# Optimization experiments

Hardware: AMD Instinct MI355X
Metric: run time of the kernel (lower is better)

Reference implementation:

```python
import jax, jax.numpy as jnp
import numpy as np

HEADS = 8
DIM_HEAD = 32
EPS = 1e-5


def setup_inputs() -> dict:
    key = jax.random.key(0)
    ks = jax.random.split(key, 6)
    B, C, N = 2, 256, 2048
    inner = HEADS * DIM_HEAD  # 256
    return {
        "x": jax.random.normal(ks[0], (B, C, N), dtype=jnp.float32),
        "gamma": jnp.ones((C,), dtype=jnp.float32),
        "beta": jnp.zeros((C,), dtype=jnp.float32),
        "wk": jax.random.normal(ks[1], (inner, C // HEADS), dtype=jnp.float32) * 0.05,
        "wq": jax.random.normal(ks[2], (inner, C // HEADS), dtype=jnp.float32) * 0.05,
        "wv": jax.random.normal(ks[3], (inner, C // HEADS), dtype=jnp.float32) * 0.05,
        "wo": jax.random.normal(ks[4], (C, inner), dtype=jnp.float32) * 0.05,
        "bo": jnp.zeros((C,), dtype=jnp.float32),
    }


def reference(x, gamma, beta, wk, wq, wv, wo, bo):
    B, C, N = x.shape
    inner = HEADS * DIM_HEAD
    # BatchNorm1d (training mode: batch stats over B and N per channel)
    mean = jnp.mean(x, axis=(0, 2), keepdims=True)
    var = jnp.mean((x - mean) ** 2, axis=(0, 2), keepdims=True)
    xn = (x - mean) * jax.lax.rsqrt(var + EPS) * gamma[None, :, None] + beta[None, :, None]

    # grouped 1x1 conv1d (groups=HEADS): group g maps C//H input chans -> DIM_HEAD out chans
    xg = xn.reshape(B, HEADS, C // HEADS, N)

    def proj(w):
        w3 = w.reshape(HEADS, DIM_HEAD, C // HEADS)
        return jnp.einsum('hdc,bhcn->bhdn', w3, xg).reshape(B, inner, N)

    k = proj(wk)
    q = proj(wq)
    v = proj(wv)

    # faithful rearrange 'b (d h) n -> b h n d' (d outer, h inner in the channel split)
    def split_heads(t):
        return t.reshape(B, DIM_HEAD, HEADS, N).transpose(0, 2, 3, 1)  # b h n d

    # faithful q/k swap from the original: q<-split(k), k<-split(q), v<-split(v)
    qh, kh, vh = split_heads(k), split_heads(q), split_heads(v)

    scale = DIM_HEAD ** -0.5
    dots = jnp.einsum('bhid,bhjd->bhij', qh, kh) * scale  # [B,H,N,N]
    attn = jax.nn.softmax(dots, axis=-1)
    out = jnp.einsum('bhij,bhjd->bhid', attn, vh)  # [B,H,N,D]

    # rearrange 'b h n d -> b (h d) n'
    out = out.transpose(0, 1, 3, 2).reshape(B, inner, N)
    # output 1x1 conv with bias
    return jnp.einsum('oc,bcn->bon', wo, out) + bo[None, :, None]
```

## Files before the change

kernel.cpp:

```cpp
#include <hip/hip_runtime.h>

#define TID threadIdx.x

constexpr int B = 2, C = 256, N = 2048, H = 8, D = 32, BH = 16;
constexpr float EPS = 1e-5f;
constexpr float SCL2 = 0.25505654344454694f;
constexpr size_t SZ = (size_t)BH * N * D;

typedef _Float16 h8 __attribute__((ext_vector_type(8)));
typedef _Float16 h4 __attribute__((ext_vector_type(4)));
typedef __fp16 fp16x2 __attribute__((ext_vector_type(2)));
typedef float f32x4 __attribute__((ext_vector_type(4)));

__global__ __launch_bounds__(256) void k_bnstats(const float* __restrict__ x,
                                                 const float* __restrict__ gamma,
                                                 const float* __restrict__ beta,
                                                 float* __restrict__ stats) {
  int c = blockIdx.x;
  float s = 0.f, ss = 0.f;
  const float4* x4 = (const float4*)x;
  for (int k = 0; k < B; ++k) {
    const float4* p = x4 + (size_t)(k * C + c) * (N / 4);
    for (int i = TID; i < N / 4; i += 256) {
      float4 v = p[i];
      s += v.x + v.y + v.z + v.w;
      ss += v.x * v.x + v.y * v.y + v.z * v.z + v.w * v.w;
    }
  }
#pragma unroll
  for (int off = 32; off; off >>= 1) {
    s += __shfl_down(s, off);
    ss += __shfl_down(ss, off);
  }
  __shared__ float red[8];
  int w = TID >> 6;
  if ((TID & 63) == 0) { red[w] = s; red[4 + w] = ss; }
  __syncthreads();
  if (TID == 0) {
    float S = red[0] + red[1] + red[2] + red[3];
    float SS = red[4] + red[5] + red[6] + red[7];
    float mean = S * (1.f / (B * N));
    float var = SS * (1.f / (B * N)) - mean * mean;
    float a = rsqrtf(var + EPS) * gamma[c];
    stats[c] = a;
    stats[C + c] = beta[c] - mean * a;
  }
}

__global__ __launch_bounds__(256) void k_proj(const float* __restrict__ x,
    const float* __restrict__ wk, const float* __restrict__ wq,
    const float* __restrict__ wv, const float* __restrict__ stats,
    _Float16* __restrict__ qa, _Float16* __restrict__ ka, _Float16* __restrict__ va) {
  int proj = blockIdx.x >> 8;
  int rem = blockIdx.x & 255;
  int b = rem >> 7;
  int n0 = (rem & 127) * 16;
  const float* w = proj == 0 ? wk : (proj == 1 ? wq : wv);
  _Float16* out = proj == 0 ? qa : (proj == 1 ? ka : va);
  float qs = (proj == 0) ? SCL2 : 1.0f;

  __shared__ float w_t[32 * 264];
  __shared__ float xs[256 * 18];
  __shared__ float sab[512];

  sab[TID] = stats[TID];
  sab[256 + TID] = stats[256 + TID];
  {
    const float4* wr4 = (const float4*)(w + TID * 32);
#pragma unroll
    for (int p = 0; p < 8; ++p) {
      float4 v = wr4[p];
      w_t[(p * 4 + 0) * 264 + TID] = v.x;
      w_t[(p * 4 + 1) * 264 + TID] = v.y;
      w_t[(p * 4 + 2) * 264 + TID] = v.z;
      w_t[(p * 4 + 3) * 264 + TID] = v.w;
    }
  }
  __syncthreads();
#pragma unroll
  for (int p = 0; p < 4; ++p) {
    int c = p * 64 + (TID >> 2);
    int n4 = (TID & 3) * 4;
    float4 v = *(const float4*)(x + (size_t)(b * C + c) * N + n0 + n4);
    float a = sab[c], bb = sab[256 + c];
    int row = (c >> 5) + ((c & 31) << 3);
    int swz = ((row >> 4) & 3) << 2;
    float2 lo = {v.x * a + bb, v.y * a + bb};
    float2 hi = {v.z * a + bb, v.w * a + bb};
    *(float2*)&xs[row * 18 + (n4 ^ swz)] = lo;
    *(float2*)&xs[row * 18 + ((n4 + 2) ^ swz)] = hi;
  }
  __syncthreads();

  int d = TID & 31, t2 = TID >> 5;
  int g = d >> 2;
  float2 acc[8];
#pragma unroll
  for (int h = 0; h < 8; ++h) acc[h] = (float2){0.f, 0.f};
#pragma unroll
  for (int c = 0; c < 32; ++c) {
    float4 w0 = *(const float4*)&w_t[c * 264 + 8 * d];
    float4 w1 = *(const float4*)&w_t[c * 264 + 8 * d + 4];
    int row = g + 8 * c;
    int swz = ((row >> 4) & 3) << 2;
    float2 xv = *(const float2*)&xs[row * 18 + ((t2 * 2) ^ swz)];
    acc[0].x += w0.x * xv.x; acc[0].y += w0.x * xv.y;
    acc[1].x += w0.y * xv.x; acc[1].y += w0.y * xv.y;
    acc[2].x += w0.z * xv.x; acc[2].y += w0.z * xv.y;
    acc[3].x += w0.w * xv.x; acc[3].y += w0.w * xv.y;
    acc[4].x += w1.x * xv.x; acc[4].y += w1.x * xv.y;
    acc[5].x += w1.y * xv.x; acc[5].y += w1.y * xv.y;
    acc[6].x += w1.z * xv.x; acc[6].y += w1.z * xv.y;
    acc[7].x += w1.w * xv.x; acc[7].y += w1.w * xv.y;
  }
  int n = n0 + t2 * 2;
  if (proj < 2) {
#pragma unroll
    for (int h = 0; h < 8; ++h) {
      size_t o = ((size_t)((b * 8 + h) * N) + n) * D + d;
      out[o] = (_Float16)(acc[h].x * qs);
      out[o + D] = (_Float16)(acc[h].y * qs);
    }
  } else {
#pragma unroll
    for (int h = 0; h < 8; ++h) {
      size_t o = ((size_t)((b * 8 + h) * D) + d) * N + n;
      out[o] = (_Float16)acc[h].x;
      out[o + 1] = (_Float16)acc[h].y;
    }
  }
}

__global__ __launch_bounds__(256, 4) void k_attn(
    const _Float16* __restrict__ qa, const _Float16* __restrict__ ka,
    const _Float16* __restrict__ va, float* __restrict__ op,
    float* __restrict__ mp, float* __restrict__ lp) {
  int bid = blockIdx.x;
  int r = bid & 7;
  int q = bid >> 3;
  int js = q >> 6;
  int bh = r * 2 + ((q >> 5) & 1);
  int rb = q & 31;
  constexpr int nst = 8;

  int w = TID >> 6;
  int lane = TID & 63;
  int il = lane & 15;
  int g = lane >> 4;

  __shared__ char Kc[2][8192];
  __shared__ char Vc[2][8192];

  int n_q = rb * 64 + w * 16 + il;
  h8 qf = *(const h8*)(qa + ((size_t)bh * N + n_q) * D + g * 8);

  f32x4 accO0[2], accO1[2];
#pragma unroll
  for (int dh = 0; dh < 2; ++dh) {
    accO0[dh] = (f32x4){0.f, 0.f, 0.f, 0.f};
    accO1[dh] = (f32x4){0.f, 0.f, 0.f, 0.f};
  }
  float m0 = -3.0e38f, l0 = 0.f, m1 = -3.0e38f, l1 = 0.f;

  int kj = TID >> 2, kc = TID & 3;
  int pk = ((kj >> 5) * 2 + ((kj >> 2) & 1)) * 16 + ((kj >> 3) & 3) * 4 + (kj & 3);
  const _Float16* kbase = ka + ((size_t)bh * N + (size_t)js * 1024 + kj) * D + kc * 8;
  int kdst = (pk * 64 + kc * 16) ^ ((pk & 3) << 4);
  int vd = TID >> 3, vc = TID & 7;
  const _Float16* vbase = va + ((size_t)bh * D + vd) * N + (size_t)js * 1024 + vc * 8;
  int vdst = (vd * 128 + vc * 16) ^ ((vd & 7) << 4) ^ (((vd >> 3) & 3) << 5);

  h8 k0 = *(const h8*)kbase;
  h8 k1 = *(const h8*)(kbase + 64 * D);
  h8 v0 = *(const h8*)vbase;
  h8 v1 = *(const h8*)(vbase + 64);
  *(h8*)(Kc[0] + kdst) = k0;
  *(h8*)(Kc[0] + 4096 + kdst) = k1;
  *(h8*)(Vc[0] + vdst) = v0;
  *(h8*)(Vc[0] + 4096 + vdst) = v1;
  __syncthreads();

  auto tile = [&](int cur, int u, float& m, float& l, f32x4* accO) {
    const char* Kt = Kc[cur] + u * 4096;
    const char* Vt = Vc[cur] + u * 4096;
    float pv[4][4];
    float tmax = -3.0e38f;
#pragma unroll
    for (int jt = 0; jt < 4; ++jt) {
      int krow = jt * 16 + il;
      h8 kf = *(const h8*)(Kt + ((krow * 64 + g * 16) ^ ((krow & 3) << 4)));
      f32x4 accS = (f32x4){0.f, 0.f, 0.f, 0.f};
      accS = __builtin_amdgcn_mfma_f32_16x16x32_f16(kf, qf, accS, 0, 0, 0);
#pragma unroll
      for (int e = 0; e < 4; ++e) {
        pv[jt][e] = accS[e];
        tmax = fmaxf(tmax, accS[e]);
      }
    }
    tmax = fmaxf(tmax, __shfl_xor(tmax, 16));
    tmax = fmaxf(tmax, __shfl_xor(tmax, 32));
    if (__any(tmax > m)) {
      float mn = fmaxf(m, tmax);
      float corr = exp2f(m - mn);
      l *= corr;
#pragma unroll
      for (int dh = 0; dh < 2; ++dh)
#pragma unroll
        for (int e = 0; e < 4; ++e) accO[dh][e] *= corr;
      m = mn;
    }
    float ls = 0.f;
#pragma unroll
    for (int jt = 0; jt < 4; ++jt)
#pragma unroll
      for (int e = 0; e < 4; ++e) {
        float pe = exp2f(pv[jt][e] - m);
        pv[jt][e] = pe;
        ls += pe;
      }
    ls += __shfl_xor(ls, 16);
    ls += __shfl_xor(ls, 32);
    l += ls;

#pragma unroll
    for (int jb = 0; jb < 2; ++jb) {
      union { h8 v; fp16x2 p[4]; } u2;
      u2.p[0] = __builtin_amdgcn_cvt_pkrtz(pv[2 * jb][0], pv[2 * jb][1]);
      u2.p[1] = __builtin_amdgcn_cvt_pkrtz(pv[2 * jb][2], pv[2 * jb][3]);
      u2.p[2] = __builtin_amdgcn_cvt_pkrtz(pv[2 * jb + 1][0], pv[2 * jb + 1][1]);
      u2.p[3] = __builtin_amdgcn_cvt_pkrtz(pv[2 * jb + 1][2], pv[2 * jb + 1][3]);
#pragma unroll
      for (int dh = 0; dh < 2; ++dh) {
        int vrow = dh * 16 + il;
        int vaddr = (vrow * 128 + jb * 64 + g * 16) ^ ((vrow & 7) << 4) ^
                    (((vrow >> 3) & 3) << 5);
        h8 vf = *(const h8*)(Vt + vaddr);
        accO[dh] = __builtin_amdgcn_mfma_f32_16x16x32_f16(vf, u2.v, accO[dh], 0, 0, 0);
      }
    }
  };

#pragma unroll
  for (int st = 0; st < nst; ++st) {
    int cur = st & 1;
    bool more = (st + 1 < nst);
    if (more) {
      k0 = *(const h8*)(kbase + (size_t)(st + 1) * 128 * D);
      k1 = *(const h8*)(kbase + (size_t)(st + 1) * 128 * D + 64 * D);
      v0 = *(const h8*)(vbase + (st + 1) * 128);
      v1 = *(const h8*)(vbase + (st + 1) * 128 + 64);
    }

    tile(cur, 0, m0, l0, accO0);
    tile(cur, 1, m1, l1, accO1);

    if (more) {
      *(h8*)(Kc[cur ^ 1] + kdst) = k0;
      *(h8*)(Kc[cur ^ 1] + 4096 + kdst) = k1;
      *(h8*)(Vc[cur ^ 1] + vdst) = v0;
      *(h8*)(Vc[cur ^ 1] + 4096 + vdst) = v1;
      __syncthreads();
    }
  }

  float m = fmaxf(m0, m1);
  float c0 = exp2f(m0 - m), c1 = exp2f(m1 - m);
  float l = l0 * c0 + l1 * c1;
  f32x4 accO[2];
#pragma unroll
  for (int dh = 0; dh < 2; ++dh)
#pragma unroll
    for (int e = 0; e < 4; ++e)
      accO[dh][e] = accO0[dh][e] * c0 + accO1[dh][e] * c1;

  int b = bh >> 3, h = bh & 7;
  size_t obase = ((size_t)((js * 2 + b) * N) + n_q) * C + h * 32;
#pragma unroll
  for (int dh = 0; dh < 2; ++dh) {
    float4 o4 = {accO[dh][0], accO[dh][1], accO[dh][2], accO[dh][3]};
    *(float4*)(op + obase + dh * 16 + g * 4) = o4;
  }
  if (g == 0) {
    size_t idx = (size_t)(js * BH + bh) * N + n_q;
    mp[idx] = m;
    lp[idx] = l;
  }
}

__global__ __launch_bounds__(256) void k_final(const float* __restrict__ op,
    const float* __restrict__ mp, const float* __restrict__ lp,
    const float* __restrict__ wo, const float* __restrict__ bo,
    float* __restrict__ out) {
  __shared__ _Float16 woh[32 * 256];
  __shared__ _Float16 wol[32 * 256];
  __shared__ _Float16 as_[32 * 256];
  __shared__ float cwa[8 * 32], cwb[8 * 32];
  __shared__ float bos[32];
  int nt = blockIdx.x & 63, oq = (blockIdx.x >> 6) & 7, b = blockIdx.x >> 9;
  int n0 = nt * 32, o0 = oq * 32;

  {
    int h = TID >> 5, n_l = TID & 31;
    size_t i0 = (size_t)(b * 8 + h) * N + n0 + n_l;
    size_t i1 = (size_t)(BH + b * 8 + h) * N + n0 + n_l;
    float m0 = mp[i0], m1 = mp[i1];
    float mg = fmaxf(m0, m1);
    float w0 = exp2f(m0 - mg), w1 = exp2f(m1 - mg);
    float inv = 1.f / (w0 * lp[i0] + w1 * lp[i1]);
    cwa[TID] = w0 * inv;
    cwb[TID] = w1 * inv;
  }
  if (TID < 32) bos[TID] = bo[o0 + TID];
  {
    int cc = TID & 63;
    int ob = TID >> 6;
#pragma unroll
    for (int p = 0; p < 8; ++p) {
      int o = ob + p * 4;
      float4 v = ((const float4*)wo)[(o0 + o) * 64 + cc];
      _Float16 h0 = (_Float16)v.x, h1 = (_Float16)v.y,
               h2c = (_Float16)v.z, h3 = (_Float16)v.w;
      h4 hi = {h0, h1, h2c, h3};
      h4 lo = {(_Float16)(v.x - (float)h0), (_Float16)(v.y - (float)h1),
               (_Float16)(v.z - (float)h2c), (_Float16)(v.w - (float)h3)};
      int byte = (o * 512 + cc * 8) ^ ((o & 7) << 4);
      *(h4*)((char*)woh + byte) = hi;
      *(h4*)((char*)wol + byte) = lo;
    }
  }
  __syncthreads();
  {
    int cc = TID & 63;
    int h = cc >> 3;
    int nb = TID >> 6;
#pragma unroll
    for (int p = 0; p < 8; ++p) {
      int n = nb + p * 4;
      float4 v0 = *(const float4*)(op + ((size_t)(b * N) + n0 + n) * C + cc * 4);
      float4 v1 = *(const float4*)(op + ((size_t)((2 + b) * N) + n0 + n) * C + cc * 4);
      float ca = cwa[h * 32 + n], cb = cwb[h * 32 + n];
      h4 av = {(_Float16)(ca * v0.x + cb * v1.x), (_Float16)(ca * v0.y + cb * v1.y),
               (_Float16)(ca * v0.z + cb * v1.z), (_Float16)(ca * v0.w + cb * v1.w)};
      int byte = (n * 512 + cc * 8) ^ ((n & 7) << 4);
      *(h4*)((char*)as_ + byte) = av;
    }
  }
  __syncthreads();

  int w = TID >> 6, lane = TID & 63, il = lane & 15, g = lane >> 4;
  int ow = (w & 1) * 16, nw = (w >> 1) * 16;
  f32x4 acc = (f32x4){0.f, 0.f, 0.f, 0.f};
#pragma unroll
  for (int ks = 0; ks < 8; ++ks) {
    int abyte = ((nw + il) * 512 + ks * 64 + g * 16) ^ ((il & 7) << 4);
    h8 bf = *(const h8*)((char*)as_ + abyte);
    int wbyte = ((ow + il) * 512 + ks * 64 + g * 16) ^ ((il & 7) << 4);
    h8 ah = *(const h8*)((char*)woh + wbyte);
    h8 al = *(const h8*)((char*)wol + wbyte);
    acc = __builtin_amdgcn_mfma_f32_16x16x32_f16(ah, bf, acc, 0, 0, 0);
    acc = __builtin_amdgcn_mfma_f32_16x16x32_f16(al, bf, acc, 0, 0, 0);
  }
  int n = n0 + nw + il;
#pragma unroll
  for (int r = 0; r < 4; ++r) {
    int o_l = ow + g * 4 + r;
    out[(size_t)(b * C + o0 + o_l) * N + n] = acc[r] + bos[o_l];
  }
}

extern "C" void kernel_launch(void* const* d_in, const int* in_sizes, int n_in,
                              void* d_out, int out_size, void* d_ws, size_t ws_size,
                              hipStream_t stream) {
  const float* x = (const float*)d_in[0];
  const float* gamma = (const float*)d_in[1];
  const float* beta = (const float*)d_in[2];
  const float* wk = (const float*)d_in[3];
  const float* wq = (const float*)d_in[4];
  const float* wv = (const float*)d_in[5];
  const float* wo = (const float*)d_in[6];
  const float* bo = (const float*)d_in[7];
  float* out = (float*)d_out;
  float* ws = (float*)d_ws;

  float* stats = ws;
  _Float16* qa = (_Float16*)(ws + 1024);
  _Float16* ka = qa + SZ;
  _Float16* va = ka + SZ;
  float* op = (float*)(va + SZ);
  float* mp = op + 2 * SZ;
  float* lp = mp + 2 * (size_t)BH * N;

  k_bnstats<<<256, 256, 0, stream>>>(x, gamma, beta, stats);
  k_proj<<<768, 256, 0, stream>>>(x, wk, wq, wv, stats, qa, ka, va);
  k_attn<<<1024, 256, 0, stream>>>(qa, ka, va, op, mp, lp);
  k_final<<<1024, 256, 0, stream>>>(op, mp, lp, wo, bo, out);
}
```

Before: 58.73 us.

## Process two query groups per wave in attention to reuse K/V tiles

Each wave now handles 32 query rows (two 16-row groups) instead of 16, so the attention kernel launches half as many blocks and every K and V fragment read from LDS feeds two MFMAs. The two in-block key-half accumulators with their final merge are replaced by per-group running softmax state. This cuts the per-query cost of global K/V loads and LDS reads, but raises register pressure and lowers the occupancy bound from 4 to 2 blocks per CU.

After: 60.10 us. 2.3% more time.

```diff
diff --git a/kernel.cpp b/kernel.cpp
--- a/kernel.cpp
+++ b/kernel.cpp
@@ -131,16 +131,16 @@
   }
 }
 
-__global__ __launch_bounds__(256, 4) void k_attn(
+__global__ __launch_bounds__(256, 2) void k_attn(
     const _Float16* __restrict__ qa, const _Float16* __restrict__ ka,
     const _Float16* __restrict__ va, float* __restrict__ op,
     float* __restrict__ mp, float* __restrict__ lp) {
   int bid = blockIdx.x;
   int r = bid & 7;
   int q = bid >> 3;
-  int js = q >> 6;
-  int bh = r * 2 + ((q >> 5) & 1);
-  int rb = q & 31;
+  int js = q >> 5;
+  int bh = r * 2 + ((q >> 4) & 1);
+  int rb = q & 15;
   constexpr int nst = 8;
 
   int w = TID >> 6;
@@ -151,16 +151,17 @@
   __shared__ char Kc[2][8192];
   __shared__ char Vc[2][8192];
 
-  int n_q = rb * 64 + w * 16 + il;
-  h8 qf = *(const h8*)(qa + ((size_t)bh * N + n_q) * D + g * 8);
-
-  f32x4 accO0[2], accO1[2];
-#pragma unroll
-  for (int dh = 0; dh < 2; ++dh) {
-    accO0[dh] = (f32x4){0.f, 0.f, 0.f, 0.f};
-    accO1[dh] = (f32x4){0.f, 0.f, 0.f, 0.f};
-  }
-  float m0 = -3.0e38f, l0 = 0.f, m1 = -3.0e38f, l1 = 0.f;
+  int nq0 = rb * 128 + w * 32 + il;
+  h8 qf[2];
+  qf[0] = *(const h8*)(qa + ((size_t)bh * N + nq0) * D + g * 8);
+  qf[1] = *(const h8*)(qa + ((size_t)bh * N + nq0 + 16) * D + g * 8);
+
+  f32x4 accO[2][2];
+#pragma unroll
+  for (int grp = 0; grp < 2; ++grp)
+#pragma unroll
+    for (int dh = 0; dh < 2; ++dh) accO[grp][dh] = (f32x4){0.f, 0.f, 0.f, 0.f};
+  float m[2] = {-3.0e38f, -3.0e38f}, l[2] = {0.f, 0.f};
 
   int kj = TID >> 2, kc = TID & 3;
   int pk = ((kj >> 5) * 2 + ((kj >> 2) & 1)) * 16 + ((kj >> 3) & 3) * 4 + (kj & 3);
@@ -180,62 +181,77 @@
   *(h8*)(Vc[0] + 4096 + vdst) = v1;
   __syncthreads();
 
-  auto tile = [&](int cur, int u, float& m, float& l, f32x4* accO) {
+  auto tile = [&](int cur, int u) {
     const char* Kt = Kc[cur] + u * 4096;
     const char* Vt = Vc[cur] + u * 4096;
-    float pv[4][4];
-    float tmax = -3.0e38f;
+    float pv[2][4][4];
+    float tmax[2] = {-3.0e38f, -3.0e38f};
 #pragma unroll
     for (int jt = 0; jt < 4; ++jt) {
       int krow = jt * 16 + il;
       h8 kf = *(const h8*)(Kt + ((krow * 64 + g * 16) ^ ((krow & 3) << 4)));
-      f32x4 accS = (f32x4){0.f, 0.f, 0.f, 0.f};
-      accS = __builtin_amdgcn_mfma_f32_16x16x32_f16(kf, qf, accS, 0, 0, 0);
-#pragma unroll
-      for (int e = 0; e < 4; ++e) {
-        pv[jt][e] = accS[e];
-        tmax = fmaxf(tmax, accS[e]);
+#pragma unroll
+      for (int grp = 0; grp < 2; ++grp) {
+        f32x4 accS = (f32x4){0.f, 0.f, 0.f, 0.f};
+        accS = __builtin_amdgcn_mfma_f32_16x16x32_f16(kf, qf[grp], accS, 0, 0, 0);
+#pragma unroll
+        for (int e = 0; e < 4; ++e) {
+          pv[grp][jt][e] = accS[e];
+          tmax[grp] = fmaxf(tmax[grp], accS[e]);
+        }
       }
     }
-    tmax = fmaxf(tmax, __shfl_xor(tmax, 16));
-    tmax = fmaxf(tmax, __shfl_xor(tmax, 32));
-    if (__any(tmax > m)) {
-      float mn = fmaxf(m, tmax);
-      float corr = exp2f(m - mn);
-      l *= corr;
-#pragma unroll
-      for (int dh = 0; dh < 2; ++dh)
-#pragma unroll
-        for (int e = 0; e < 4; ++e) accO[dh][e] *= corr;
-      m = mn;
-    }
-    float ls = 0.f;
-#pragma unroll
-    for (int jt = 0; jt < 4; ++jt)
-#pragma unroll
-      for (int e = 0; e < 4; ++e) {
-        float pe = exp2f(pv[jt][e] - m);
-        pv[jt][e] = pe;
-        ls += pe;
+#pragma unroll
+    for (int grp = 0; grp < 2; ++grp) {
+      float tm = tmax[grp];
+      tm = fmaxf(tm, __shfl_xor(tm, 16));
+      tm = fmaxf(tm, __shfl_xor(tm, 32));
+      if (__any(tm > m[grp])) {
+        float mn = fmaxf(m[grp], tm);
+        float corr = exp2f(m[grp] - mn);
+        l[grp] *= corr;
+#pragma unroll
+        for (int dh = 0; dh < 2; ++dh)
+#pragma unroll
+          for (int e = 0; e < 4; ++e) accO[grp][dh][e] *= corr;
+        m[grp] = mn;
       }
-    ls += __shfl_xor(ls, 16);
-    ls += __shfl_xor(ls, 32);
-    l += ls;
+      float ls = 0.f;
+#pragma unroll
+      for (int jt = 0; jt < 4; ++jt)
+#pragma unroll
+        for (int e = 0; e < 4; ++e) {
+          float pe = exp2f(pv[grp][jt][e] - m[grp]);
+          pv[grp][jt][e] = pe;
+          ls += pe;
+        }
+      ls += __shfl_xor(ls, 16);
+      ls += __shfl_xor(ls, 32);
+      l[grp] += ls;
+    }
 
 #pragma unroll
     for (int jb = 0; jb < 2; ++jb) {
-      union { h8 v; fp16x2 p[4]; } u2;
-      u2.p[0] = __builtin_amdgcn_cvt_pkrtz(pv[2 * jb][0], pv[2 * jb][1]);
-      u2.p[1] = __builtin_amdgcn_cvt_pkrtz(pv[2 * jb][2], pv[2 * jb][3]);
-      u2.p[2] = __builtin_amdgcn_cvt_pkrtz(pv[2 * jb + 1][0], pv[2 * jb + 1][1]);
-      u2.p[3] = __builtin_amdgcn_cvt_pkrtz(pv[2 * jb + 1][2], pv[2 * jb + 1][3]);
+      h8 pf[2];
+#pragma unroll
+      for (int grp = 0; grp < 2; ++grp) {
+        union { h8 v; fp16x2 p[4]; } u2;
+        u2.p[0] = __builtin_amdgcn_cvt_pkrtz(pv[grp][2 * jb][0], pv[grp][2 * jb][1]);
+        u2.p[1] = __builtin_amdgcn_cvt_pkrtz(pv[grp][2 * jb][2], pv[grp][2 * jb][3]);
+        u2.p[2] = __builtin_amdgcn_cvt_pkrtz(pv[grp][2 * jb + 1][0], pv[grp][2 * jb + 1][1]);
+        u2.p[3] = __builtin_amdgcn_cvt_pkrtz(pv[grp][2 * jb + 1][2], pv[grp][2 * jb + 1][3]);
+        pf[grp] = u2.v;
+      }
 #pragma unroll
       for (int dh = 0; dh < 2; ++dh) {
         int vrow = dh * 16 + il;
         int vaddr = (vrow * 128 + jb * 64 + g * 16) ^ ((vrow & 7) << 4) ^
                     (((vrow >> 3) & 3) << 5);
         h8 vf = *(const h8*)(Vt + vaddr);
-        accO[dh] = __builtin_amdgcn_mfma_f32_16x16x32_f16(vf, u2.v, accO[dh], 0, 0, 0);
+#pragma unroll
+        for (int grp = 0; grp < 2; ++grp)
+          accO[grp][dh] =
+              __builtin_amdgcn_mfma_f32_16x16x32_f16(vf, pf[grp], accO[grp][dh], 0, 0, 0);
       }
     }
   };
@@ -251,8 +267,8 @@
       v1 = *(const h8*)(vbase + (st + 1) * 128 + 64);
     }
 
-    tile(cur, 0, m0, l0, accO0);
-    tile(cur, 1, m1, l1, accO1);
+    tile(cur, 0);
+    tile(cur, 1);
 
     if (more) {
       *(h8*)(Kc[cur ^ 1] + kdst) = k0;
@@ -263,27 +279,21 @@
     }
   }
 
-  float m = fmaxf(m0, m1);
-  float c0 = exp2f(m0 - m), c1 = exp2f(m1 - m);
-  float l = l0 * c0 + l1 * c1;
-  f32x4 accO[2];
-#pragma unroll
-  for (int dh = 0; dh < 2; ++dh)
-#pragma unroll
-    for (int e = 0; e < 4; ++e)
-      accO[dh][e] = accO0[dh][e] * c0 + accO1[dh][e] * c1;
-
   int b = bh >> 3, h = bh & 7;
-  size_t obase = ((size_t)((js * 2 + b) * N) + n_q) * C + h * 32;
-#pragma unroll
-  for (int dh = 0; dh < 2; ++dh) {
-    float4 o4 = {accO[dh][0], accO[dh][1], accO[dh][2], accO[dh][3]};
-    *(float4*)(op + obase + dh * 16 + g * 4) = o4;
-  }
-  if (g == 0) {
-    size_t idx = (size_t)(js * BH + bh) * N + n_q;
-    mp[idx] = m;
-    lp[idx] = l;
+#pragma unroll
+  for (int grp = 0; grp < 2; ++grp) {
+    int nq = nq0 + grp * 16;
+    size_t obase = ((size_t)((js * 2 + b) * N) + nq) * C + h * 32;
+#pragma unroll
+    for (int dh = 0; dh < 2; ++dh) {
+      float4 o4 = {accO[grp][dh][0], accO[grp][dh][1], accO[grp][dh][2], accO[grp][dh][3]};
+      *(float4*)(op + obase + dh * 16 + g * 4) = o4;
+    }
+    if (g == 0) {
+      size_t idx = (size_t)(js * BH + bh) * N + nq;
+      mp[idx] = m[grp];
+      lp[idx] = l[grp];
+    }
   }
 }
 
@@ -392,6 +402,6 @@
 
   k_bnstats<<<256, 256, 0, stream>>>(x, gamma, beta, stats);
   k_proj<<<768, 256, 0, stream>>>(x, wk, wq, wv, stats, qa, ka, va);
-  k_attn<<<1024, 256, 0, stream>>>(qa, ka, va, op, mp, lp);
+  k_attn<<<512, 256, 0, stream>>>(qa, ka, va, op, mp, lp);
   k_final<<<1024, 256, 0, stream>>>(op, mp, lp, wo, bo, out);
 }
```
